# Optimization experiments

Hardware: AMD Instinct MI355X
Metric: run time of the kernel (lower is better)

The kernel has to match this reference:

```python
import jax, jax.numpy as jnp
import numpy as np

B, NUM_REF, FDIM, H, W, D = 2, 3, 256, 64, 64, 10
GAMMA = 0.5


def setup_inputs() -> dict:
    key = jax.random.key(0)
    k1, k2, k3, k4 = jax.random.split(key, 4)
    ref = jax.random.normal(k1, (B, NUM_REF, FDIM, H, W), jnp.float32)
    target = jax.random.normal(k2, (B, FDIM, H, W), jnp.float32)
    # one-hot reference labels, class axis = 2, per docstring
    lab = jax.random.randint(k3, (B, NUM_REF, H, W), 0, D)
    ref_label = jax.nn.one_hot(lab, D, axis=2, dtype=jnp.float32)  # (B,NUM_REF,D,H,W)
    target_label = jax.random.randint(k4, (B, H, W), 0, D)
    return {
        "ref": ref,
        "target": target,
        "ref_label": ref_label,
        "target_label": target_label,
        "unused1": 0,
        "unused2": 0,
    }


def reference(ref, target, ref_label, target_label, unused1, unused2):
    b, n, f, h, w = ref.shape
    # similarity: (B, num_ref*H*W, H*W)
    r = jnp.transpose(ref, (0, 1, 3, 4, 2)).reshape(b, n * h * w, f)
    t = target.reshape(b, f, h * w)
    sim = jnp.einsum('brf,bft->brt', r, t)
    sim = jax.nn.softmax(sim, axis=1)  # softmax over reference pixels
    # label propagation: (B, d, H*W)
    d = ref_label.shape[2]
    rl = jnp.transpose(ref_label, (0, 2, 1, 3, 4)).reshape(b, d, n * h * w)
    pred = jnp.einsum('bdr,brt->bdt', rl, sim)  # (B, d, Nt)
    # flatten to (B*H*W, d), matching torch permute(0,2,3,1).reshape(-1,c)
    pred = jnp.transpose(pred, (0, 2, 1)).reshape(-1, d)
    tl = target_label.reshape(-1)
    log_p = jax.nn.log_softmax(pred, axis=-1)
    log_pt = jnp.take_along_axis(log_p, tl[:, None], axis=1)[:, 0]  # (B*H*W,)
    ce = -jnp.mean(log_pt)  # nn.NLLLoss default mean -> scalar
    focal_term = (1.0 - jnp.exp(log_pt)) ** GAMMA  # per-pixel
    loss = jnp.mean(focal_term * ce)  # vector * scalar, then mean
    return loss
```

## Files before the change

kernel.cpp:

```cpp
#include <hip/hip_runtime.h>
#include <hip/hip_bf16.h>
#include <stdint.h>
#include <stddef.h>

#define B_    2
#define NREF  3
#define FDIM  256
#define HW    4096
#define DCLS  10
#define RTOT  12288
#define TT    128
#define RR    64
#define RS    8
#define RPB   1536
#define NCH   24
#define NPIX  8192
#define LOG2E 1.44269504f
#define C0f   (-144.269504f)
#define SAQ   21.1666667f
#define SC2   (LOG2E / (SAQ * SAQ))

typedef __attribute__((ext_vector_type(8))) short bf16x8;
typedef __attribute__((ext_vector_type(4))) float f32x4;
typedef __attribute__((ext_vector_type(4))) int i32x4;
typedef __attribute__((ext_vector_type(4))) unsigned int u32x4;

__device__ __forceinline__ unsigned short f2bf(float x) {
  union { float f; unsigned u; } v; v.f = x;
  unsigned r = v.u + 0x7fffu + ((v.u >> 16) & 1u);
  return (unsigned short)(r >> 16);
}
__device__ __forceinline__ unsigned cvtpk(float a, float b) {
  unsigned r;
  asm("v_cvt_pk_bf16_f32 %0, %1, %2" : "=v"(r) : "v"(a), "v"(b));
  return r;
}
__device__ __forceinline__ void async16(const void* g, void* l) {
  __builtin_amdgcn_global_load_lds(
      (const __attribute__((address_space(1))) void*)g,
      (__attribute__((address_space(3))) void*)l, 16, 0, 0);
}
__device__ __forceinline__ unsigned oh2(unsigned word, int d) {
  return ((word & 255u) == (unsigned)d ? 0x3F80u : 0u) |
         (((word >> 8) & 255u) == (unsigned)d ? 0x3F800000u : 0u);
}
__device__ __forceinline__ int q8(float v) {
  v = fminf(fmaxf(v, -127.f), 127.f);
  return (int)rintf(v);
}

__global__ __launch_bounds__(256) void k_pre(const float* __restrict__ ref,
                                             const float* __restrict__ tgt,
                                             const float* __restrict__ rl,
                                             char* __restrict__ outb,
                                             unsigned char* __restrict__ lab8) {
  const int tid = threadIdx.x;
  if (blockIdx.x < 1024) {
    const int row = blockIdx.x * 32 + (tid & 31);
    const int q = tid >> 5;
    const float* src;
    if (row < B_ * RTOT) {
      const int b = row / RTOT, rr2 = row % RTOT;
      src = ref + ((size_t)(b * NREF + (rr2 >> 12)) * FDIM) * HW + (rr2 & 4095);
    } else {
      const int r2 = row - B_ * RTOT;
      src = tgt + ((size_t)(r2 >> 12) * FDIM) * HW + (r2 & 4095);
    }
    char* dst = outb + (size_t)row * 256;
    const int sw = (row & 7) << 4;
#pragma unroll
    for (int ci = 0; ci < 2; ++ci) {
      const int c16 = q * 2 + ci;
      int qv[16];
#pragma unroll
      for (int j = 0; j < 16; ++j)
        qv[j] = q8(src[(size_t)(c16 * 16 + j) * HW] * SAQ);
      u32x4 u;
#pragma unroll
      for (int g = 0; g < 4; ++g)
        u[g] = (unsigned)(qv[g * 4] & 255) | ((unsigned)(qv[g * 4 + 1] & 255) << 8) |
               ((unsigned)(qv[g * 4 + 2] & 255) << 16) | ((unsigned)(qv[g * 4 + 3] & 255) << 24);
      *(u32x4*)(dst + ((c16 * 16) ^ sw)) = u;
    }
  } else {
    const int idx = (blockIdx.x - 1024) * 256 + tid;
    if (idx >= B_ * RTOT) return;
    const int b = idx / RTOT, r = idx % RTOT;
    const float* p = rl + ((size_t)((b * NREF + (r >> 12)) * DCLS)) * HW + (r & 4095);
    int v = 0;
#pragma unroll
    for (int d = 1; d < DCLS; ++d)
      if (p[(size_t)d * HW] > 0.5f) v = d;
    lab8[idx] = (unsigned char)v;
  }
}

__global__ __launch_bounds__(256, 2) void k_main(const char* __restrict__ refb,
                                                 const char* __restrict__ tgtb,
                                                 const unsigned char* __restrict__ lab8,
                                                 float* __restrict__ pred) {
  __shared__ __align__(16) char Ash[2][RR * 256];

  const int tid = threadIdx.x;
  const int lane = tid & 63;
  const int w = tid >> 6;
  const int l15 = lane & 15, l4 = lane >> 4;
  const int rh = w >> 1, th = w & 1;
  const int swz = (l15 & 7) << 4;

  const int bid = blockIdx.x;
  const int rs = bid & 7;
  const int tb = (bid >> 3) & 31;
  const int b  = bid >> 8;

  i32x4 bfr[4][4];
  {
    const char* base = tgtb + ((size_t)(b * HW + tb * TT + th * 64)) * 256;
#pragma unroll
    for (int nt = 0; nt < 4; ++nt) {
      const char* rp = base + (size_t)((nt * 16 + l15) * 256);
#pragma unroll
      for (int ks = 0; ks < 4; ++ks)
        bfr[nt][ks] = *(const i32x4*)(rp + ((ks * 64 + l4 * 16) ^ swz));
    }
  }

  f32x4 pacc[4];
#pragma unroll
  for (int i = 0; i < 4; ++i) pacc[i] = f32x4{0.f, 0.f, 0.f, 0.f};

  const char* Asrc = refb + ((size_t)(b * RTOT + rs * RPB)) * 256;

  const char* ap00 = &Ash[0][(rh * 32 +  0 + l15) * 256 + ((     l4 * 16) ^ swz)];
  const char* ap01 = &Ash[0][(rh * 32 +  0 + l15) * 256 + ((64 + l4 * 16) ^ swz)];
  const char* ap10 = &Ash[0][(rh * 32 + 16 + l15) * 256 + ((     l4 * 16) ^ swz)];
  const char* ap11 = &Ash[0][(rh * 32 + 16 + l15) * 256 + ((64 + l4 * 16) ^ swz)];

  auto stage = [&](const char* s, char* dbuf) {
#pragma unroll
    for (int i2 = 0; i2 < 4; ++i2) {
      const int seg = i2 * 4 + w;
      async16(s + seg * 1024 + lane * 16, dbuf + seg * 1024);
    }
  };
  auto qk = [&](i32x4 (&acc)[2][4], const int OFS) {
#pragma unroll
    for (int i2 = 0; i2 < 2; ++i2)
#pragma unroll
      for (int j = 0; j < 4; ++j) acc[i2][j] = i32x4{0, 0, 0, 0};
    __builtin_amdgcn_s_setprio(1);
#pragma unroll
    for (int ks = 0; ks < 4; ++ks) {
      const int ko = OFS + (ks >> 1) * 128;
      const i32x4 af0 = *(const i32x4*)(((ks & 1) ? ap01 : ap00) + ko);
      const i32x4 af1 = *(const i32x4*)(((ks & 1) ? ap11 : ap10) + ko);
#pragma unroll
      for (int nt = 0; nt < 4; ++nt)
        acc[0][nt] = __builtin_amdgcn_mfma_i32_16x16x64_i8(
            af0, bfr[nt][ks], acc[0][nt], 0, 0, 0);
#pragma unroll
      for (int nt = 0; nt < 4; ++nt)
        acc[1][nt] = __builtin_amdgcn_mfma_i32_16x16x64_i8(
            af1, bfr[nt][ks], acc[1][nt], 0, 0, 0);
    }
    __builtin_amdgcn_s_setprio(0);
  };
  auto pv = [&](const i32x4 (&acc)[2][4], unsigned la, unsigned lb2) {
    union { bf16x8 v; unsigned u[4]; } lf;
    lf.u[0] = oh2(la, l15);        lf.u[1] = oh2(la >> 16, l15);
    lf.u[2] = oh2(lb2, l15);       lf.u[3] = oh2(lb2 >> 16, l15);
#pragma unroll
    for (int nt = 0; nt < 4; ++nt) {
      const i32x4 a0 = acc[0][nt], a1 = acc[1][nt];
      float p0 = __builtin_amdgcn_exp2f(__builtin_fmaf((float)a0[0], SC2, C0f));
      float p1 = __builtin_amdgcn_exp2f(__builtin_fmaf((float)a0[1], SC2, C0f));
      float p2 = __builtin_amdgcn_exp2f(__builtin_fmaf((float)a0[2], SC2, C0f));
      float p3 = __builtin_amdgcn_exp2f(__builtin_fmaf((float)a0[3], SC2, C0f));
      float p4 = __builtin_amdgcn_exp2f(__builtin_fmaf((float)a1[0], SC2, C0f));
      float p5 = __builtin_amdgcn_exp2f(__builtin_fmaf((float)a1[1], SC2, C0f));
      float p6 = __builtin_amdgcn_exp2f(__builtin_fmaf((float)a1[2], SC2, C0f));
      float p7 = __builtin_amdgcn_exp2f(__builtin_fmaf((float)a1[3], SC2, C0f));
      union { bf16x8 v; unsigned u[4]; } pf;
      pf.u[0] = cvtpk(p0, p1); pf.u[1] = cvtpk(p2, p3);
      pf.u[2] = cvtpk(p4, p5); pf.u[3] = cvtpk(p6, p7);
      pacc[nt] = __builtin_amdgcn_mfma_f32_16x16x32_bf16(lf.v, pf.v, pacc[nt], 0, 0, 0);
    }
  };

  i32x4 acc[2][4];
  const unsigned char* lbp = lab8 + b * RTOT + rs * RPB + rh * 32 + l4 * 4;
  const char* Acur = Asrc + 2 * (RR * 256);

  unsigned la_p = *(const unsigned*)lbp;
  unsigned lb_p = *(const unsigned*)(lbp + 16);
  lbp += RR;
  stage(Asrc, &Ash[0][0]);
  __syncthreads();
  stage(Asrc + RR * 256, &Ash[1][0]);
  qk(acc, 0);

#pragma unroll 1
  for (int i = 0; i < 11; ++i) {
    {
      __syncthreads();
      const unsigned la_n = *(const unsigned*)lbp;
      const unsigned lb_n = *(const unsigned*)(lbp + 16);
      lbp += RR;
      stage(Acur, &Ash[0][0]); Acur += RR * 256;
      pv(acc, la_p, lb_p);
      qk(acc, 16384);
      la_p = la_n; lb_p = lb_n;
    }
    {
      __syncthreads();
      const unsigned la_n = *(const unsigned*)lbp;
      const unsigned lb_n = *(const unsigned*)(lbp + 16);
      lbp += RR;
      stage(Acur, &Ash[1][0]); Acur += RR * 256;
      pv(acc, la_p, lb_p);
      qk(acc, 0);
      la_p = la_n; lb_p = lb_n;
    }
  }
  {
    __syncthreads();
    const unsigned la_n = *(const unsigned*)lbp;
    const unsigned lb_n = *(const unsigned*)(lbp + 16);
    pv(acc, la_p, lb_p);
    qk(acc, 16384);
    pv(acc, la_n, lb_n);
  }

  __syncthreads();
  float* sc = (float*)&Ash[0][0];
  if (rh == 1) {
#pragma unroll
    for (int nt = 0; nt < 4; ++nt)
      *(f32x4*)&sc[((th * 64 + lane) * 4 + nt) * 4] = pacc[nt];
  }
  __syncthreads();
  if (rh == 0) {
#pragma unroll
    for (int nt = 0; nt < 4; ++nt) {
      pacc[nt] += *(const f32x4*)&sc[((th * 64 + lane) * 4 + nt) * 4];
      const int t = th * 64 + nt * 16 + l15;
      const size_t o = (((size_t)(rs * B_ + b)) * HW + (size_t)tb * TT + t) * 16 + l4 * 4;
      *(f32x4*)&pred[o] = pacc[nt];
    }
  }
}

__global__ __launch_bounds__(256) void k_epi(const float* __restrict__ pred,
                                             const int* __restrict__ tl,
                                             float* __restrict__ red) {
  const int idx = blockIdx.x * 256 + threadIdx.x;
  const int b = idx >> 12, t = idx & 4095;
  union { f32x4 v[3]; float f[12]; } S;
  S.v[0] = f32x4{0.f, 0.f, 0.f, 0.f};
  S.v[1] = f32x4{0.f, 0.f, 0.f, 0.f};
  S.v[2] = f32x4{0.f, 0.f, 0.f, 0.f};
#pragma unroll
  for (int r = 0; r < RS; ++r) {
    const f32x4* p = (const f32x4*)&pred[(((size_t)(r * B_ + b)) * HW + t) * 16];
    S.v[0] += p[0]; S.v[1] += p[1]; S.v[2] += p[2];
  }
  float T = 0.f;
#pragma unroll
  for (int d = 0; d < DCLS; ++d) T += S.f[d];
  const float inv = 1.f / T;
  const int lb = tl[idx];
  float se = 0.f, zt = 0.f;
#pragma unroll
  for (int d = 0; d < DCLS; ++d) {
    const float z = S.f[d] * inv;
    se += __expf(z);
    if (d == lb) zt = z;
  }
  const float logpt = zt - __logf(se);
  const float pt = __expf(zt) / se;
  const float focal = sqrtf(fmaxf(1.f - pt, 0.f));

  float lp = logpt, fo = focal;
#pragma unroll
  for (int off = 32; off; off >>= 1) {
    lp += __shfl_down(lp, off);
    fo += __shfl_down(fo, off);
  }
  __shared__ float rb_[8];
  const int lane = threadIdx.x & 63, wv = threadIdx.x >> 6;
  if (lane == 0) { rb_[wv] = lp; rb_[4 + wv] = fo; }
  __syncthreads();
  if (threadIdx.x == 0) {
    red[blockIdx.x * 2 + 0] = rb_[0] + rb_[1] + rb_[2] + rb_[3];
    red[blockIdx.x * 2 + 1] = rb_[4] + rb_[5] + rb_[6] + rb_[7];
  }
}

__global__ void k_fin(const float* __restrict__ red, float* __restrict__ out) {
  const int tid = threadIdx.x;
  float lp = 0.f, fo = 0.f;
  if (tid < 32) { lp = red[tid * 2]; fo = red[tid * 2 + 1]; }
#pragma unroll
  for (int off = 16; off; off >>= 1) {
    lp += __shfl_down(lp, off);
    fo += __shfl_down(fo, off);
  }
  if (tid == 0) {
    const float ce = -lp / (float)NPIX;
    out[0] = ce * (fo / (float)NPIX);
  }
}

extern "C" void kernel_launch(void* const* d_in, const int* in_sizes, int n_in,
                              void* d_out, int out_size, void* d_ws, size_t ws_size,
                              hipStream_t stream)
{
  const float* ref  = (const float*)d_in[0];
  const float* tgt  = (const float*)d_in[1];
  const float* rl   = (const float*)d_in[2];
  const int*   tlab = (const int*)d_in[3];
  float* out = (float*)d_out;

  char* ws = (char*)d_ws;
  char* refb = ws;
  char* tgtb = ws + (size_t)24576 * 256;
  unsigned char* lab8 = (unsigned char*)(ws + 8388608);
  float* pred = (float*)(ws + 8388608 + 32768);
  float* red  = (float*)(ws + 8388608 + 32768 + 4194304);

  k_pre<<<1120, 256, 0, stream>>>(ref, tgt, rl, refb, lab8);
  k_main<<<512, 256, 0, stream>>>(refb, tgtb, lab8, pred);
  k_epi<<<32, 256, 0, stream>>>(pred, tlab, red);
  k_fin<<<1, 64, 0, stream>>>(red, out);
}
```

Measured before the change: 51.50 us.

## Triple-buffer reference tiles with manual vmcnt waits and preload labels to LDS

```diff
diff --git a/kernel.cpp b/kernel.cpp
--- a/kernel.cpp
+++ b/kernel.cpp
@@ -49,6 +49,14 @@
   return (int)rintf(v);
 }
 
+#define WAITV(N) asm volatile("s_waitcnt vmcnt(" #N ")" ::: "memory")
+#define RAWBAR()                                  \
+  do {                                            \
+    asm volatile("" ::: "memory");                \
+    __builtin_amdgcn_s_barrier();                 \
+    asm volatile("" ::: "memory");                \
+  } while (0)
+
 __global__ __launch_bounds__(256) void k_pre(const float* __restrict__ ref,
                                              const float* __restrict__ tgt,
                                              const float* __restrict__ rl,
@@ -99,7 +107,8 @@
                                                  const char* __restrict__ tgtb,
                                                  const unsigned char* __restrict__ lab8,
                                                  float* __restrict__ pred) {
-  __shared__ __align__(16) char Ash[2][RR * 256];
+  __shared__ __align__(16) char Ash[3][RR * 256];
+  __shared__ __align__(16) char Lsh[2048];
 
   const int tid = threadIdx.x;
   const int lane = tid & 63;
@@ -188,47 +197,55 @@
   };
 
   i32x4 acc[2][4];
-  const unsigned char* lbp = lab8 + b * RTOT + rs * RPB + rh * 32 + l4 * 4;
+  const char* lq = &Lsh[rh * 32 + l4 * 4];
+  auto lab_lo = [&](int c) { return *(const unsigned*)(lq + c * 64); };
+  auto lab_hi = [&](int c) { return *(const unsigned*)(lq + c * 64 + 16); };
+
+  {
+    const unsigned char* lbase = lab8 + b * RTOT + rs * RPB;
+    if (tid < 96)
+      *(u32x4*)&Lsh[tid * 16] = *(const u32x4*)(lbase + tid * 16);
+  }
+  stage(Asrc, &Ash[0][0]);
+  stage(Asrc + RR * 256, &Ash[1][0]);
   const char* Acur = Asrc + 2 * (RR * 256);
-
-  unsigned la_p = *(const unsigned*)lbp;
-  unsigned lb_p = *(const unsigned*)(lbp + 16);
-  lbp += RR;
-  stage(Asrc, &Ash[0][0]);
   __syncthreads();
-  stage(Asrc + RR * 256, &Ash[1][0]);
+
+  stage(Acur, &Ash[2][0]); Acur += RR * 256;
   qk(acc, 0);
 
 #pragma unroll 1
-  for (int i = 0; i < 11; ++i) {
+  for (int i = 0; i < 7; ++i) {
+    const int c0 = 3 * i + 1;
     {
-      __syncthreads();
-      const unsigned la_n = *(const unsigned*)lbp;
-      const unsigned lb_n = *(const unsigned*)(lbp + 16);
-      lbp += RR;
+      WAITV(4); RAWBAR();
       stage(Acur, &Ash[0][0]); Acur += RR * 256;
-      pv(acc, la_p, lb_p);
+      pv(acc, lab_lo(c0 - 1), lab_hi(c0 - 1));
       qk(acc, 16384);
-      la_p = la_n; lb_p = lb_n;
     }
     {
-      __syncthreads();
-      const unsigned la_n = *(const unsigned*)lbp;
-      const unsigned lb_n = *(const unsigned*)(lbp + 16);
-      lbp += RR;
+      WAITV(4); RAWBAR();
       stage(Acur, &Ash[1][0]); Acur += RR * 256;
-      pv(acc, la_p, lb_p);
+      pv(acc, lab_lo(c0), lab_hi(c0));
+      qk(acc, 32768);
+    }
+    {
+      WAITV(4); RAWBAR();
+      stage(Acur, &Ash[2][0]); Acur += RR * 256;
+      pv(acc, lab_lo(c0 + 1), lab_hi(c0 + 1));
       qk(acc, 0);
-      la_p = la_n; lb_p = lb_n;
     }
   }
   {
-    __syncthreads();
-    const unsigned la_n = *(const unsigned*)lbp;
-    const unsigned lb_n = *(const unsigned*)(lbp + 16);
-    pv(acc, la_p, lb_p);
+    WAITV(4); RAWBAR();
+    pv(acc, lab_lo(21), lab_hi(21));
     qk(acc, 16384);
-    pv(acc, la_n, lb_n);
+  }
+  {
+    WAITV(0); RAWBAR();
+    pv(acc, lab_lo(22), lab_hi(22));
+    qk(acc, 32768);
+    pv(acc, lab_lo(23), lab_hi(23));
   }
 
   __syncthreads();
```

Result: no change. 51.79 us (+0.6%).
